# Kernel optimization log

Hardware: AMD Instinct MI355X
Metric: run time of the kernel (lower is better)

The kernel has to match this reference:

```python
import jax, jax.numpy as jnp
import numpy as np

B, T, C = 4, 2048, 2048
H, HS = 16, 128  # num_heads, head_size; H*HS == C


def setup_inputs() -> dict:
    key = jax.random.key(0)
    k1, k2, k3, k4 = jax.random.split(key, 4)
    x = jax.random.normal(k1, (B, T, C), dtype=jnp.float32)
    # nn.Linear weights are [out, in]; scale ~ kaiming-uniform-ish
    w_qkv = jax.random.normal(k2, (3 * C, C), dtype=jnp.float32) * (1.0 / np.sqrt(C))
    w_proj = jax.random.normal(k3, (C, C), dtype=jnp.float32) * (1.0 / np.sqrt(C))
    b_proj = jax.random.normal(k4, (C,), dtype=jnp.float32) * 0.01
    return {"x": x, "w_qkv": w_qkv, "w_proj": w_proj, "b_proj": b_proj}


def reference(x, w_qkv, w_proj, b_proj):
    Bq, Tq, Cq = x.shape
    qkv = jnp.einsum("btc,dc->btd", x, w_qkv)  # [B,T,3C]
    q, k, v = jnp.split(qkv, 3, axis=2)
    # [B,T,C] -> [B,H,T,hs]
    q = q.reshape(Bq, Tq, H, HS).transpose(0, 2, 1, 3)
    k = k.reshape(Bq, Tq, H, HS).transpose(0, 2, 1, 3)
    v = v.reshape(Bq, Tq, H, HS).transpose(0, 2, 1, 3)
    scale = 1.0 / np.sqrt(HS)
    scores = jnp.einsum("bhqd,bhkd->bhqk", q, k) * scale  # [B,H,T,T]
    causal = jnp.tril(jnp.ones((Tq, Tq), dtype=bool))
    scores = jnp.where(causal, scores, jnp.finfo(scores.dtype).min)
    attn = jax.nn.softmax(scores, axis=-1)
    out = jnp.einsum("bhqk,bhkd->bhqd", attn, v)  # [B,H,T,hs]
    out = out.transpose(0, 2, 1, 3).reshape(Bq, Tq, Cq)
    out = jnp.einsum("btc,dc->btd", out, w_proj) + b_proj
    return out
```

## Files before the change

kernel.cpp:

```cpp
#include <hip/hip_runtime.h>

#define Tq 2048
#define Cq 2048
#define Hn 16
#define HSz 128
#define Bq 4
#define SCALE_QK 0.08838834764831845f

typedef __bf16 bf16x8 __attribute__((ext_vector_type(8)));
typedef float f32x4 __attribute__((ext_vector_type(4)));
typedef unsigned short u16;
typedef u16 u16x4 __attribute__((ext_vector_type(4)));

__device__ __forceinline__ u16 f2bf(float f) {
  unsigned u = __builtin_bit_cast(unsigned, f);
  u += 0x7FFFu + ((u >> 16) & 1u);
  return (u16)(u >> 16);
}

__device__ __forceinline__ bf16x8 ld_frag(const void* p) {
  bf16x8 v; __builtin_memcpy(&v, p, 16); return v;
}

__device__ __forceinline__ void glds16(void* lds, const void* g) {
  __builtin_amdgcn_global_load_lds(
      (const __attribute__((address_space(1))) void*)g,
      (__attribute__((address_space(3))) void*)lds, 16, 0, 0);
}

__global__ void cvt_bf16(const float* __restrict__ in, u16* __restrict__ out, int n) {
  int i = (blockIdx.x * 256 + threadIdx.x) * 4;
  if (i >= n) return;
  f32x4 v; __builtin_memcpy(&v, in + i, 16);
  u16x4 o;
  o[0] = f2bf(v[0]); o[1] = f2bf(v[1]); o[2] = f2bf(v[2]); o[3] = f2bf(v[3]);
  __builtin_memcpy(out + i, &o, 8);
}


#define LDA(s, mh) do { \
  _Pragma("unroll") for (int mi2_ = 0; mi2_ < 4; ++mi2_) \
  _Pragma("unroll") for (int kk_ = 0; kk_ < 2; ++kk_) { \
    const int row_ = (mh)*128 + wm*64 + mi2_*16 + lr; \
    af[mi2_*2+kk_] = ld_frag(AsB + (s)*32768 + row_*128 + ((kk_*64 + lg*16) ^ swz)); \
  } } while(0)

#define LDB(s, nh, BF) do { \
  _Pragma("unroll") for (int nf2_ = 0; nf2_ < 2; ++nf2_) \
  _Pragma("unroll") for (int kk_ = 0; kk_ < 2; ++kk_) { \
    const int row_ = (nh)*128 + wn*32 + nf2_*16 + lr; \
    BF[nf2_*2+kk_] = ld_frag(BsB + (s)*32768 + row_*128 + ((kk_*64 + lg*16) ^ swz)); \
  } } while(0)

#define QUAD(mh, nh, BF) do { \
  _Pragma("unroll") for (int mi2_ = 0; mi2_ < 4; ++mi2_) \
  _Pragma("unroll") for (int nf2_ = 0; nf2_ < 2; ++nf2_) \
  _Pragma("unroll") for (int kk_ = 0; kk_ < 2; ++kk_) \
    acc[(mh)*4+mi2_][(nh)*2+nf2_] = __builtin_amdgcn_mfma_f32_16x16x32_bf16( \
        af[mi2_*2+kk_], BF[nf2_*2+kk_], acc[(mh)*4+mi2_][(nh)*2+nf2_], 0, 0, 0); \
  } while(0)

#define STAGE_A(s, mh, k0) do { \
    u16* dst_ = Asu + (s)*16384 + (mh)*8192; \
    const u16* sp_ = A + (size_t)(m0 + (mh)*64 + arow0) * K + (k0) + srcE; \
    glds16(dst_ + w*512, sp_); \
    glds16(dst_ + (8+w)*512, sp_ + (size_t)128 * K); \
  } while(0)

#define STAGE_B(s, nh, k0) do { \
    u16* dst_ = Bsu + (s)*16384 + (nh)*8192; \
    glds16(dst_ + w*512,     Bm + (size_t)(n0 + (nh)*32 + brow0) * K + (k0) + srcE); \
    glds16(dst_ + (8+w)*512, Bm + (size_t)(n0 + (nh)*32 + brow1) * K + (k0) + srcE); \
  } while(0)

#define SYNC_MFMA(QPART) do { \
    asm volatile("s_barrier" ::: "memory"); \
    __builtin_amdgcn_s_setprio(1); \
    QPART; \
    __builtin_amdgcn_s_setprio(0); \
    asm volatile("s_barrier" ::: "memory"); \
  } while(0)

template <int EPI>
__global__ __launch_bounds__(512)
void gemm256(const u16* __restrict__ A, const u16* __restrict__ Bm, int K,
             u16* __restrict__ qout, u16* __restrict__ kout, u16* __restrict__ vtout,
             float* __restrict__ fout, const float* __restrict__ bias) {
  __shared__ u16 As2[2 * 256 * 64];
  __shared__ u16 Bs2[2 * 256 * 64];
  const int tid = threadIdx.x;
  const int w = tid >> 6, l = tid & 63;
  const int wm = w >> 2, wn = w & 3;
  const int lr = l & 15, lg = l >> 4;
  const int swz = (lr & 7) << 4;

  const int nwg = gridDim.x * gridDim.y;
  int ow = blockIdx.y * gridDim.x + blockIdx.x;
  ow = (ow & 7) * (nwg >> 3) + (ow >> 3);
  const int bx = ow % gridDim.x, by = ow / gridDim.x;
  const int m0 = by * 256, n0 = bx * 256;

  const int r0 = w * 8 + (l >> 3);
  const int arow0 = r0;
  const int brow0 = (r0 >> 5) * 64 + (r0 & 31);
  const int brow1 = (((r0 + 64) >> 5) & 3) * 64 + (r0 & 31);
  const int srcE = ((l & 7) ^ (l >> 3)) << 3;

  u16* Asu = As2; u16* Bsu = Bs2;
  const char* AsB = (const char*)As2;
  const char* BsB = (const char*)Bs2;

  f32x4 acc[8][4];
  const f32x4 fz = {0.f, 0.f, 0.f, 0.f};
#pragma unroll
  for (int i = 0; i < 8; ++i)
#pragma unroll
    for (int j = 0; j < 4; ++j) acc[i][j] = fz;

  bf16x8 af[8], bf0[4], bf1[4];

  STAGE_A(0, 0, 0);  STAGE_B(0, 0, 0);  STAGE_B(0, 1, 0);  STAGE_A(0, 1, 0);
  STAGE_A(1, 0, 64); STAGE_B(1, 0, 64); STAGE_B(1, 1, 64);
  asm volatile("s_waitcnt vmcnt(6)" ::: "memory");
  asm volatile("s_barrier" ::: "memory");

  const int NP = K >> 7;
#pragma unroll 1
  for (int t = 0; t < NP; ++t) {
    const bool lastp = (t == NP - 1);
    const int kA = (t + 1) << 7;

    LDA(0, 0); LDB(0, 0, bf0);
    STAGE_A(1, 1, (t << 7) + 64);
    SYNC_MFMA(QUAD(0, 0, bf0));
    LDB(0, 1, bf1);
    if (!lastp) STAGE_A(0, 0, kA);
    SYNC_MFMA(QUAD(0, 1, bf1));
    LDA(0, 1);
    if (!lastp) STAGE_B(0, 0, kA);
    SYNC_MFMA(QUAD(1, 1, bf1));
    if (!lastp) { STAGE_B(0, 1, kA); asm volatile("s_waitcnt vmcnt(6)" ::: "memory"); }
    else        {                    asm volatile("s_waitcnt vmcnt(0)" ::: "memory"); }
    SYNC_MFMA(QUAD(1, 0, bf0));

    LDA(1, 0); LDB(1, 0, bf0);
    if (!lastp) STAGE_A(0, 1, kA);
    SYNC_MFMA(QUAD(0, 0, bf0));
    LDB(1, 1, bf1);
    if (!lastp) STAGE_A(1, 0, kA + 64);
    SYNC_MFMA(QUAD(0, 1, bf1));
    LDA(1, 1);
    if (!lastp) STAGE_B(1, 0, kA + 64);
    SYNC_MFMA(QUAD(1, 1, bf1));
    if (!lastp) { STAGE_B(1, 1, kA + 64); asm volatile("s_waitcnt vmcnt(6)" ::: "memory"); }
    else        {                         asm volatile("s_waitcnt vmcnt(0)" ::: "memory"); }
    SYNC_MFMA(QUAD(1, 0, bf0));
  }

  if constexpr (EPI == 0) {
#pragma unroll
    for (int mi = 0; mi < 8; ++mi) {
      const int trow = m0 + wm * 128 + mi * 16 + lg * 4;
      const int bb = trow >> 11, tt0 = trow & 2047;
#pragma unroll
      for (int nf = 0; nf < 4; ++nf) {
        const int d = n0 + wn * 64 + nf * 16 + lr;
        const int part = d >> 11;
        const int dd = d & 2047;
        const int hh = dd >> 7, hs = dd & 127;
        if (part == 2) {
          u16x4 pk;
          pk[0] = f2bf(acc[mi][nf][0]); pk[1] = f2bf(acc[mi][nf][1]);
          pk[2] = f2bf(acc[mi][nf][2]); pk[3] = f2bf(acc[mi][nf][3]);
          size_t off = ((size_t)(bb * Hn + hh) * HSz + hs) * Tq + tt0;
          __builtin_memcpy(&vtout[off], &pk, 8);
        } else {
          u16* dst = (part == 0) ? qout : kout;
#pragma unroll
          for (int rr = 0; rr < 4; ++rr) {
            size_t off = ((size_t)(bb * Hn + hh) * Tq + (tt0 + rr)) * HSz + hs;
            dst[off] = f2bf(acc[mi][nf][rr]);
          }
        }
      }
    }
  } else {
#pragma unroll
    for (int mi = 0; mi < 8; ++mi) {
      const int trow = m0 + wm * 128 + mi * 16 + lg * 4;
#pragma unroll
      for (int nf = 0; nf < 4; ++nf) {
        const int d = n0 + wn * 64 + nf * 16 + lr;
        const float bv = bias[d];
#pragma unroll
        for (int rr = 0; rr < 4; ++rr)
          fout[(size_t)(trow + rr) * Cq + d] = acc[mi][nf][rr] + bv;
      }
    }
  }
}

#define KVB 64
__global__ __launch_bounds__(256, 2)
void attn_fwd(const u16* __restrict__ qb, const u16* __restrict__ kb,
              const u16* __restrict__ vtb, u16* __restrict__ ob) {
  __shared__ u16 Ks[2 * KVB * HSz];
  __shared__ u16 Vs[2 * HSz * KVB];
  __shared__ u16 Ps[4 * 32 * 32];

  const int tid = threadIdx.x;
  const int w = tid >> 6, l = tid & 63;
  const int lr = l & 15, lg = l >> 4;
  const int bh = blockIdx.x, jj0 = blockIdx.y;
  const int b = bh >> 4, h = bh & 15;

  const u16* qp = qb + (size_t)bh * Tq * HSz;
  const u16* kp = kb + (size_t)bh * Tq * HSz;
  const u16* vp = vtb + (size_t)bh * HSz * Tq;

#pragma unroll 1
  for (int pass = 0; pass < 2; ++pass) {
    const int qt = pass ? (15 - jj0) : jj0;
    const int q0 = qt * 128;

    bf16x8 qf[2][4];
#pragma unroll
    for (int mi = 0; mi < 2; ++mi)
#pragma unroll
      for (int kk = 0; kk < 4; ++kk) {
        int row = q0 + w * 32 + mi * 16 + lr;
        qf[mi][kk] = ld_frag(qp + (size_t)row * HSz + kk * 32 + lg * 8);
      }

    const f32x4 fz = {0.f, 0.f, 0.f, 0.f};
    f32x4 o[2][8];
    float mrow[2][4], lrow[2][4];
#pragma unroll
    for (int mi = 0; mi < 2; ++mi) {
#pragma unroll
      for (int nj = 0; nj < 8; ++nj) o[mi][nj] = fz;
#pragma unroll
      for (int rr = 0; rr < 4; ++rr) { mrow[mi][rr] = -1e30f; lrow[mi][rr] = 0.f; }
    }

    const int nt = 2 * (qt + 1);

    auto stage = [&](int t, int buf) {
      const int kv0 = t * KVB;
      u16* Kb = &Ks[buf * (KVB * HSz)];
      u16* Vb = &Vs[buf * (HSz * KVB)];
#pragma unroll
      for (int i = 0; i < 4; ++i) {
        int c = w * 4 + i;
        {
          int r = c * 4 + lg;
          int cb = (lr * 16) ^ ((r & 7) << 4);
          glds16(&Kb[c * 512], (const char*)(kp + (size_t)(kv0 + r) * HSz) + cb);
        }
        {
          int r = c * 8 + (l >> 3);
          int cb = ((l & 7) * 16) ^ ((r & 7) << 4);
          glds16(&Vb[c * 512], (const char*)(vp + (size_t)r * Tq + kv0) + cb);
        }
      }
    };

    stage(0, 0);
#pragma unroll 1
    for (int t = 0; t < nt; ++t) {
      const int buf = t & 1;
      if (t + 1 < nt) {
        stage(t + 1, buf ^ 1);
        asm volatile("s_waitcnt vmcnt(8)\ns_barrier" ::: "memory");
      } else {
        asm volatile("s_waitcnt vmcnt(0)\ns_barrier" ::: "memory");
      }
      const u16* Ksb = &Ks[buf * (KVB * HSz)];
      const u16* Vsb = &Vs[buf * (HSz * KVB)];
      const int kv0 = t * KVB;

      f32x4 s[2][4];
#pragma unroll
      for (int mi = 0; mi < 2; ++mi)
#pragma unroll
        for (int nj = 0; nj < 4; ++nj) s[mi][nj] = fz;
#pragma unroll
      for (int kk = 0; kk < 4; ++kk) {
        bf16x8 kf[4];
#pragma unroll
        for (int nj = 0; nj < 4; ++nj) {
          int row = nj * 16 + lr;
          int cb = (kk * 64 + lg * 16) ^ ((row & 7) << 4);
          kf[nj] = ld_frag((const char*)Ksb + row * 256 + cb);
        }
        __builtin_amdgcn_s_setprio(1);
#pragma unroll
        for (int mi = 0; mi < 2; ++mi)
#pragma unroll
          for (int nj = 0; nj < 4; ++nj)
            s[mi][nj] = __builtin_amdgcn_mfma_f32_16x16x32_bf16(qf[mi][kk], kf[nj], s[mi][nj], 0, 0, 0);
        __builtin_amdgcn_s_setprio(0);
      }

      const bool diag = (t >= nt - 2);
      float corr[2][4];
      bool grew = false;
#pragma unroll
      for (int mi = 0; mi < 2; ++mi) {
#pragma unroll
        for (int rr = 0; rr < 4; ++rr) {
          const int qrow = q0 + w * 32 + mi * 16 + lg * 4 + rr;
          float pm = -1e30f;
#pragma unroll
          for (int nj = 0; nj < 4; ++nj) {
            float v = s[mi][nj][rr] * SCALE_QK;
            if (diag && (kv0 + nj * 16 + lr) > qrow) v = -1e30f;
            s[mi][nj][rr] = v;
            pm = fmaxf(pm, v);
          }
          pm = fmaxf(pm, __shfl_xor(pm, 1));
          pm = fmaxf(pm, __shfl_xor(pm, 2));
          pm = fmaxf(pm, __shfl_xor(pm, 4));
          pm = fmaxf(pm, __shfl_xor(pm, 8));
          float mo = mrow[mi][rr];
          float mn = fmaxf(mo, pm);
          corr[mi][rr] = __expf(mo - mn);
          grew |= (pm > mo);
          mrow[mi][rr] = mn;
          float rs = 0.f;
#pragma unroll
          for (int nj = 0; nj < 4; ++nj) {
            float p = __expf(s[mi][nj][rr] - mn);
            s[mi][nj][rr] = p;
            rs += p;
          }
          rs += __shfl_xor(rs, 1);
          rs += __shfl_xor(rs, 2);
          rs += __shfl_xor(rs, 4);
          rs += __shfl_xor(rs, 8);
          lrow[mi][rr] = lrow[mi][rr] * corr[mi][rr] + rs;
        }
      }
      if (__any(grew)) {
#pragma unroll
        for (int mi = 0; mi < 2; ++mi)
#pragma unroll
          for (int nj = 0; nj < 8; ++nj)
#pragma unroll
            for (int rr = 0; rr < 4; ++rr) o[mi][nj][rr] *= corr[mi][rr];
      }

      char* pw = (char*)Ps + w * 2048;
#pragma unroll
      for (int kk = 0; kk < 2; ++kk) {
#pragma unroll
        for (int mi = 0; mi < 2; ++mi)
#pragma unroll
          for (int jj = 0; jj < 2; ++jj) {
            int nj = kk * 2 + jj;
#pragma unroll
            for (int rr = 0; rr < 4; ++rr) {
              int prow = mi * 16 + lg * 4 + rr;
              int pcb = (jj * 16 + lr) * 2;
              *(u16*)(pw + ((prow * 64 + pcb) ^ ((prow & 7) << 4))) = f2bf(s[mi][nj][rr]);
            }
          }
        bf16x8 pa[2];
#pragma unroll
        for (int mi = 0; mi < 2; ++mi) {
          int prow = mi * 16 + lr;
          pa[mi] = ld_frag(pw + ((prow * 64 + lg * 16) ^ ((prow & 7) << 4)));
        }
        __builtin_amdgcn_s_setprio(1);
#pragma unroll
        for (int nj = 0; nj < 8; ++nj) {
          int vrow = nj * 16 + lr;
          int cb = (kk * 64 + lg * 16) ^ ((vrow & 7) << 4);
          bf16x8 vf = ld_frag((const char*)Vsb + vrow * 128 + cb);
#pragma unroll
          for (int mi = 0; mi < 2; ++mi)
            o[mi][nj] = __builtin_amdgcn_mfma_f32_16x16x32_bf16(pa[mi], vf, o[mi][nj], 0, 0, 0);
        }
        __builtin_amdgcn_s_setprio(0);
      }

      asm volatile("s_barrier" ::: "memory");
    }

#pragma unroll
    for (int mi = 0; mi < 2; ++mi)
#pragma unroll
      for (int rr = 0; rr < 4; ++rr) {
        int trow = q0 + w * 32 + mi * 16 + lg * 4 + rr;
        float inv = 1.f / lrow[mi][rr];
#pragma unroll
        for (int nj = 0; nj < 8; ++nj) {
          int d = nj * 16 + lr;
          ob[((size_t)b * Tq + trow) * Cq + h * HSz + d] = f2bf(o[mi][nj][rr] * inv);
        }
      }
  }
}

extern "C" void kernel_launch(void* const* d_in, const int* in_sizes, int n_in,
                              void* d_out, int out_size, void* d_ws, size_t ws_size,
                              hipStream_t stream) {
  const float* x = (const float*)d_in[0];
  const float* w_qkv = (const float*)d_in[1];
  const float* w_proj = (const float*)d_in[2];
  const float* b_proj = (const float*)d_in[3];
  float* out = (float*)d_out;

  char* ws = (char*)d_ws;
  u16* xb     = (u16*)(ws);
  u16* wqkvb  = (u16*)(ws + (size_t)33554432);
  u16* wprojb = (u16*)(ws + (size_t)58720256);
  u16* qbp    = (u16*)(ws + (size_t)67108864);
  u16* kbp    = (u16*)(ws + (size_t)100663296);
  u16* vtbp   = (u16*)(ws + (size_t)134217728);
  (void)in_sizes; (void)n_in; (void)out_size; (void)ws_size;

  cvt_bf16<<<16384, 256, 0, stream>>>(x, xb, 16777216);
  cvt_bf16<<<12288, 256, 0, stream>>>(w_qkv, wqkvb, 12582912);
  cvt_bf16<<<4096, 256, 0, stream>>>(w_proj, wprojb, 4194304);

  gemm256<0><<<dim3(24, 32), 512, 0, stream>>>(xb, wqkvb, 2048, qbp, kbp, vtbp, nullptr, nullptr);

  attn_fwd<<<dim3(64, 8), 256, 0, stream>>>(qbp, kbp, vtbp, xb);

  gemm256<1><<<dim3(8, 32), 512, 0, stream>>>(xb, wprojb, 2048, nullptr, nullptr, nullptr, out, b_proj);
}
```

Before: 470.0 us.

## Restructure GEMM main loop into four phases with peeled final iteration

Merges pairs of MFMA quads into single barrier-protected phases, cutting barriers per k-iteration from sixteen to eight. Global-to-LDS staging is regrouped and the vmcnt waits are retuned to match. The last k-iteration is peeled out so the loop body has no per-stage lastp branches. The risk is that fewer sync points change how loads overlap compute, and wrong wait counts could cause LDS data hazards.

```diff
diff --git a/kernel.cpp b/kernel.cpp
--- a/kernel.cpp
+++ b/kernel.cpp
@@ -73,13 +73,15 @@
     glds16(dst_ + (8+w)*512, Bm + (size_t)(n0 + (nh)*32 + brow1) * K + (k0) + srcE); \
   } while(0)
 
-#define SYNC_MFMA(QPART) do { \
+#define SYNC_MFMA(...) do { \
     asm volatile("s_barrier" ::: "memory"); \
     __builtin_amdgcn_s_setprio(1); \
-    QPART; \
+    __VA_ARGS__; \
     __builtin_amdgcn_s_setprio(0); \
     asm volatile("s_barrier" ::: "memory"); \
   } while(0)
+
+#define FENCE(n) asm volatile("s_waitcnt vmcnt(" #n ")" ::: "memory")
 
 template <int EPI>
 __global__ __launch_bounds__(512)
@@ -119,42 +121,50 @@
 
   bf16x8 af[8], bf0[4], bf1[4];
 
-  STAGE_A(0, 0, 0);  STAGE_B(0, 0, 0);  STAGE_B(0, 1, 0);  STAGE_A(0, 1, 0);
+  STAGE_A(0, 0, 0);  STAGE_B(0, 0, 0);  STAGE_B(0, 1, 0);
+  STAGE_A(0, 1, 0);
   STAGE_A(1, 0, 64); STAGE_B(1, 0, 64); STAGE_B(1, 1, 64);
-  asm volatile("s_waitcnt vmcnt(6)" ::: "memory");
+  FENCE(8);
   asm volatile("s_barrier" ::: "memory");
 
   const int NP = K >> 7;
 #pragma unroll 1
-  for (int t = 0; t < NP; ++t) {
-    const bool lastp = (t == NP - 1);
-    const int kA = (t + 1) << 7;
-
-    LDA(0, 0); LDB(0, 0, bf0);
-    STAGE_A(1, 1, (t << 7) + 64);
-    SYNC_MFMA(QUAD(0, 0, bf0));
-    LDB(0, 1, bf1);
-    if (!lastp) STAGE_A(0, 0, kA);
-    SYNC_MFMA(QUAD(0, 1, bf1));
+  for (int t = 0; t < NP - 1; ++t) {
+    const int kt = t << 7;
+    const int kA = kt + 128;
+
+    LDA(0, 0); LDB(0, 0, bf0); LDB(0, 1, bf1);
+    STAGE_A(1, 1, kt + 64);
+    FENCE(8);
+    SYNC_MFMA(QUAD(0, 0, bf0); QUAD(0, 1, bf1));
     LDA(0, 1);
-    if (!lastp) STAGE_B(0, 0, kA);
-    SYNC_MFMA(QUAD(1, 1, bf1));
-    if (!lastp) { STAGE_B(0, 1, kA); asm volatile("s_waitcnt vmcnt(6)" ::: "memory"); }
-    else        {                    asm volatile("s_waitcnt vmcnt(0)" ::: "memory"); }
-    SYNC_MFMA(QUAD(1, 0, bf0));
-
-    LDA(1, 0); LDB(1, 0, bf0);
-    if (!lastp) STAGE_A(0, 1, kA);
-    SYNC_MFMA(QUAD(0, 0, bf0));
-    LDB(1, 1, bf1);
-    if (!lastp) STAGE_A(1, 0, kA + 64);
-    SYNC_MFMA(QUAD(0, 1, bf1));
+    STAGE_A(0, 0, kA); STAGE_B(0, 0, kA); STAGE_B(0, 1, kA);
+    FENCE(8);
+    SYNC_MFMA(QUAD(1, 1, bf1); QUAD(1, 0, bf0));
+    LDA(1, 0); LDB(1, 0, bf0); LDB(1, 1, bf1);
+    STAGE_A(0, 1, kA);
+    FENCE(8);
+    SYNC_MFMA(QUAD(0, 0, bf0); QUAD(0, 1, bf1));
     LDA(1, 1);
-    if (!lastp) STAGE_B(1, 0, kA + 64);
-    SYNC_MFMA(QUAD(1, 1, bf1));
-    if (!lastp) { STAGE_B(1, 1, kA + 64); asm volatile("s_waitcnt vmcnt(6)" ::: "memory"); }
-    else        {                         asm volatile("s_waitcnt vmcnt(0)" ::: "memory"); }
-    SYNC_MFMA(QUAD(1, 0, bf0));
+    STAGE_A(1, 0, kA + 64); STAGE_B(1, 0, kA + 64); STAGE_B(1, 1, kA + 64);
+    FENCE(8);
+    SYNC_MFMA(QUAD(1, 1, bf1); QUAD(1, 0, bf0));
+  }
+
+  {
+    const int kt = (NP - 1) << 7;
+    LDA(0, 0); LDB(0, 0, bf0); LDB(0, 1, bf1);
+    STAGE_A(1, 1, kt + 64);
+    FENCE(8);
+    SYNC_MFMA(QUAD(0, 0, bf0); QUAD(0, 1, bf1));
+    LDA(0, 1);
+    FENCE(2);
+    SYNC_MFMA(QUAD(1, 1, bf1); QUAD(1, 0, bf0));
+    LDA(1, 0); LDB(1, 0, bf0); LDB(1, 1, bf1);
+    FENCE(0);
+    SYNC_MFMA(QUAD(0, 0, bf0); QUAD(0, 1, bf1));
+    LDA(1, 1);
+    SYNC_MFMA(QUAD(1, 1, bf1); QUAD(1, 0, bf0));
   }
 
   if constexpr (EPI == 0) {
```

Result: no change. 465.9 us (-0.9%).
